# Optimization experiments

Hardware: AMD Instinct MI355X
Metric: run time of the kernel (lower is better)

## Reference

```python
import jax, jax.numpy as jnp
import numpy as np

B, C, H, W, N = 4, 128, 240, 320, 1024
LEVEL = 8.0          # scaling[0] = 4 * img_scale with img_scale=2
E1_LAMDA = 1.0
E2_LAMDA = 2.0 / 7.0
GN_LAMDA = 0.3
EPS = 1e-9


def extract_features(f, coords):
    # f: (B,C,H,W); coords: (B,N,2) float pixel coords as (x, y)
    Bf, Cf, Hf, Wf = f.shape
    x = coords[..., 0]
    y = coords[..., 1]
    x0 = jnp.floor(x)
    y0 = jnp.floor(y)
    wx = (x - x0)[:, None, :]          # (B,1,N)
    wy = (y - y0)[:, None, :]
    x0i = jnp.clip(x0.astype(jnp.int32), 0, Wf - 1)
    x1i = jnp.clip(x0i + 1, 0, Wf - 1)
    y0i = jnp.clip(y0.astype(jnp.int32), 0, Hf - 1)
    y1i = jnp.clip(y0i + 1, 0, Hf - 1)

    def g(fm, yi, xi):                 # fm: (C,H,W), yi/xi: (N,)
        return fm[:, yi, xi]           # (C,N)

    v00 = jax.vmap(g)(f, y0i, x0i)
    v01 = jax.vmap(g)(f, y0i, x1i)
    v10 = jax.vmap(g)(f, y1i, x0i)
    v11 = jax.vmap(g)(f, y1i, x1i)
    out = (v00 * (1 - wx) * (1 - wy) + v01 * wx * (1 - wy)
           + v10 * (1 - wx) * wy + v11 * wx * wy)          # (B,C,N)
    return out.transpose(0, 2, 1).reshape(Bf * coords.shape[1], Cf)


def l2_normalize(f):
    n = jnp.linalg.norm(f, axis=1, keepdims=True)
    return f / jnp.maximum(n, 1e-12)


def torch_gradient(f):
    # central differences with edge replication; gx = d/dx (width), gy = d/dy (height)
    fpx = jnp.pad(f, ((0, 0), (0, 0), (0, 0), (1, 1)), mode='edge')
    fpy = jnp.pad(f, ((0, 0), (0, 0), (1, 1), (0, 0)), mode='edge')
    gx = 0.5 * (fpx[..., 2:] - fpx[..., :-2])
    gy = 0.5 * (fpy[..., 2:, :] - fpy[..., :-2, :])
    return gx, gy


def compute_gn_loss(f_t, fb, ub, noise):
    Bn, Nn, _ = ub.shape
    xs = (2.0 * noise - 1.0) + ub                   # uniform(-1,1) jitter
    f_s = extract_features(fb, xs)
    f_t = l2_normalize(f_t)
    f_s = l2_normalize(f_s)
    r = f_s - f_t                                   # (BN, C)
    gx, gy = torch_gradient(fb)
    Jx = extract_features(gx, xs)                   # (BN, C)
    Jy = extract_features(gy, xs)
    J = jnp.stack([Jx, Jy], axis=-1)                # (BN, C, 2)
    Hm = jnp.einsum('bci,bcj->bij', J, J) + EPS * jnp.eye(2, dtype=J.dtype)
    b = jnp.einsum('bci,bc->bi', J, r)[..., None]   # (BN, 2, 1)
    # closed-form 2x2 inverse
    a = Hm[:, 0, 0]; bb = Hm[:, 0, 1]; c = Hm[:, 1, 0]; d = Hm[:, 1, 1]
    det = a * d - bb * c
    Hinv = jnp.stack([jnp.stack([d, -bb], -1),
                      jnp.stack([-c, a], -1)], -2) / det[:, None, None]
    miu = xs.reshape(Bn * Nn, 2, 1) - Hinv @ b
    diff = (ub.reshape(Bn * Nn, 2, 1) - miu)[..., 0]          # (BN, 2)
    e1 = 0.5 * jnp.sum(jnp.einsum('bi,bij,bj->b', diff, Hm, diff))
    log_det = jnp.log(det)
    e2 = Bn * Nn * jnp.log(jnp.asarray(2.0 * np.pi, dtype=det.dtype)) - 0.5 * jnp.sum(log_det)
    e = E1_LAMDA * e1 + E2_LAMDA * e2
    return e, e1, e2


def setup_inputs() -> dict:
    key = jax.random.key(0)
    k = jax.random.split(key, 7)
    F_a = jax.random.normal(k[0], (B, C, H, W), dtype=jnp.float32)
    F_b = jax.random.normal(k[1], (B, C, H, W), dtype=jnp.float32)
    # full-resolution match coords, safely inside the map after /LEVEL
    xa = jax.random.uniform(k[2], (B, N)) * (W - 5) * LEVEL + 2 * LEVEL
    ya = jax.random.uniform(k[3], (B, N)) * (H - 5) * LEVEL + 2 * LEVEL
    xb = jax.random.uniform(k[4], (B, N)) * (W - 5) * LEVEL + 2 * LEVEL
    yb = jax.random.uniform(k[5], (B, N)) * (H - 5) * LEVEL + 2 * LEVEL
    matches_a = jnp.stack([xa, ya], axis=-1)
    matches_b = jnp.stack([xb, yb], axis=-1)
    noise = jax.random.uniform(k[6], (B, N, 2), dtype=jnp.float32)
    return {"F_a": F_a, "F_b": F_b, "matches_a": matches_a,
            "matches_b": matches_b, "noise": noise}


def reference(F_a, F_b, matches_a, matches_b, noise):
    f_t = extract_features(F_a, matches_a / LEVEL)
    e, e1, e2 = compute_gn_loss(f_t, F_b, matches_b / LEVEL, noise)
    return GN_LAMDA * e, e1, e2
```

## Files before the change

### kernel.cpp

```cpp
#include <hip/hip_runtime.h>
#include <math.h>

#define B_  4
#define C_  128
#define H_  240
#define W_  320
#define N_  1024
#define NPTS (B_ * N_)
#define HW_ (H_ * W_)

__device__ __forceinline__ float wave_reduce(float v) {
    #pragma unroll
    for (int off = 32; off > 0; off >>= 1)
        v += __shfl_xor(v, off, 64);
    return v;
}

__global__ __launch_bounds__(128) void gn_point_kernel(
    const float* __restrict__ Fa, const float* __restrict__ Fb,
    const float* __restrict__ ma, const float* __restrict__ mb,
    const float* __restrict__ noise,
    float* __restrict__ ws_e1, float* __restrict__ ws_ld)
{
    const int p = blockIdx.x;
    const int b = p >> 10;
    const int c = threadIdx.x;

    const float inv_level = 1.0f / 8.0f;
    const float xa  = ma[p * 2 + 0] * inv_level;
    const float ya  = ma[p * 2 + 1] * inv_level;
    const float ubx = mb[p * 2 + 0] * inv_level;
    const float uby = mb[p * 2 + 1] * inv_level;
    const float nx  = noise[p * 2 + 0];
    const float ny  = noise[p * 2 + 1];
    const float xs  = 2.0f * nx - 1.0f + ubx;
    const float ys  = 2.0f * ny - 1.0f + uby;

    const float ax0f = floorf(xa), ay0f = floorf(ya);
    const float awx = xa - ax0f, awy = ya - ay0f;
    int ax0 = min(max((int)ax0f, 0), W_ - 1);
    int ax1 = min(ax0 + 1, W_ - 1);
    int ay0 = min(max((int)ay0f, 0), H_ - 1);
    int ay1 = min(ay0 + 1, H_ - 1);
    const float* __restrict__ fa = Fa + ((size_t)b * C_ + c) * HW_;
    const float av00 = fa[ay0 * W_ + ax0];
    const float av01 = fa[ay0 * W_ + ax1];
    const float av10 = fa[ay1 * W_ + ax0];
    const float av11 = fa[ay1 * W_ + ax1];
    const float ft = av00 * (1.f - awx) * (1.f - awy)
                   + av01 * awx * (1.f - awy)
                   + av10 * (1.f - awx) * awy
                   + av11 * awx * awy;

    const float bx0f = floorf(xs), by0f = floorf(ys);
    const float wx = xs - bx0f, wy = ys - by0f;
    int x0 = min(max((int)bx0f, 0), W_ - 1);
    int x1 = min(x0 + 1, W_ - 1);
    int y0 = min(max((int)by0f, 0), H_ - 1);
    int y1 = min(y0 + 1, H_ - 1);
    int xm = max(x0 - 1, 0);
    int xp = min(x1 + 1, W_ - 1);
    int ym = max(y0 - 1, 0);
    int yp = min(y1 + 1, H_ - 1);
    const float* __restrict__ fb = Fb + ((size_t)b * C_ + c) * HW_;

    const float r0m = fb[y0 * W_ + xm], r00 = fb[y0 * W_ + x0];
    const float r01 = fb[y0 * W_ + x1], r0p = fb[y0 * W_ + xp];
    const float r1m = fb[y1 * W_ + xm], r10 = fb[y1 * W_ + x0];
    const float r11 = fb[y1 * W_ + x1], r1p = fb[y1 * W_ + xp];
    const float rm0 = fb[ym * W_ + x0], rm1 = fb[ym * W_ + x1];
    const float rp0 = fb[yp * W_ + x0], rp1 = fb[yp * W_ + x1];

    const float w00 = (1.f - wx) * (1.f - wy);
    const float w01 = wx * (1.f - wy);
    const float w10 = (1.f - wx) * wy;
    const float w11 = wx * wy;

    const float fs = r00 * w00 + r01 * w01 + r10 * w10 + r11 * w11;
    const float jx = 0.5f * ((r01 - r0m) * w00 + (r0p - r00) * w01
                           + (r11 - r1m) * w10 + (r1p - r10) * w11);
    const float jy = 0.5f * ((r10 - rm0) * w00 + (r11 - rm1) * w01
                           + (rp0 - r00) * w10 + (rp1 - r01) * w11);

    float vals[9];
    vals[0] = ft * ft;
    vals[1] = fs * fs;
    vals[2] = jx * fs;
    vals[3] = jx * ft;
    vals[4] = jy * fs;
    vals[5] = jy * ft;
    vals[6] = jx * jx;
    vals[7] = jx * jy;
    vals[8] = jy * jy;

    #pragma unroll
    for (int k = 0; k < 9; ++k)
        vals[k] = wave_reduce(vals[k]);

    __shared__ float sm[2][9];
    const int wid = threadIdx.x >> 6;
    const int lane = threadIdx.x & 63;
    if (lane == 0) {
        #pragma unroll
        for (int k = 0; k < 9; ++k) sm[wid][k] = vals[k];
    }
    __syncthreads();

    if (threadIdx.x == 0) {
        float s[9];
        #pragma unroll
        for (int k = 0; k < 9; ++k) s[k] = sm[0][k] + sm[1][k];

        const float nt = fmaxf(sqrtf(s[0]), 1e-12f);
        const float ns = fmaxf(sqrtf(s[1]), 1e-12f);
        const float b0 = s[2] / ns - s[3] / nt;
        const float b1 = s[4] / ns - s[5] / nt;
        const float H00 = s[6] + 1e-9f;
        const float H01 = s[7];
        const float H11 = s[8] + 1e-9f;
        const float det = H00 * H11 - H01 * H01;
        const float inv = 1.0f / det;
        const float u0 = (H11 * b0 - H01 * b1) * inv;
        const float u1 = (H00 * b1 - H01 * b0) * inv;
        const float d0 = (ubx - xs) + u0;
        const float d1 = (uby - ys) + u1;
        const float quad = d0 * (H00 * d0 + H01 * d1) + d1 * (H01 * d0 + H11 * d1);
        ws_e1[p] = 0.5f * quad;
        ws_ld[p] = logf(det);
    }
}

__global__ __launch_bounds__(256) void gn_reduce_kernel(
    const float* __restrict__ ws_e1, const float* __restrict__ ws_ld,
    float* __restrict__ out)
{
    __shared__ double sm1[256];
    __shared__ double sm2[256];
    double a1 = 0.0, a2 = 0.0;
    for (int i = threadIdx.x; i < NPTS; i += 256) {
        a1 += (double)ws_e1[i];
        a2 += (double)ws_ld[i];
    }
    sm1[threadIdx.x] = a1;
    sm2[threadIdx.x] = a2;
    __syncthreads();
    for (int s = 128; s > 0; s >>= 1) {
        if (threadIdx.x < s) {
            sm1[threadIdx.x] += sm1[threadIdx.x + s];
            sm2[threadIdx.x] += sm2[threadIdx.x + s];
        }
        __syncthreads();
    }
    if (threadIdx.x == 0) {
        const double e1 = sm1[0];
        const double sum_ld = sm2[0];
        const double log2pi = (double)logf(6.283185307179586f);
        const double e2 = (double)NPTS * log2pi - 0.5 * sum_ld;
        const double e = 1.0 * e1 + (2.0 / 7.0) * e2;
        out[0] = (float)(0.3 * e);
        out[1] = (float)e1;
        out[2] = (float)e2;
    }
}

extern "C" void kernel_launch(void* const* d_in, const int* in_sizes, int n_in,
                              void* d_out, int out_size, void* d_ws, size_t ws_size,
                              hipStream_t stream) {
    const float* Fa    = (const float*)d_in[0];
    const float* Fb    = (const float*)d_in[1];
    const float* ma    = (const float*)d_in[2];
    const float* mb    = (const float*)d_in[3];
    const float* noise = (const float*)d_in[4];
    float* out = (float*)d_out;

    float* ws_e1 = (float*)d_ws;
    float* ws_ld = ws_e1 + NPTS;

    gn_point_kernel<<<NPTS, 128, 0, stream>>>(Fa, Fb, ma, mb, noise, ws_e1, ws_ld);
    gn_reduce_kernel<<<1, 256, 0, stream>>>(ws_e1, ws_ld, out);
}
```

Measured before the change: 81.89 us.

## Map one point per wavefront with two channels per lane, drop block sync

```diff
diff --git a/kernel.cpp b/kernel.cpp
--- a/kernel.cpp
+++ b/kernel.cpp
@@ -22,102 +22,119 @@
     const float* __restrict__ noise,
     float* __restrict__ ws_e1, float* __restrict__ ws_ld)
 {
-    const int p = blockIdx.x;
+    const int wid  = threadIdx.x >> 6;
+    const int lane = threadIdx.x & 63;
+    const int p = (blockIdx.x << 1) | wid;
     const int b = p >> 10;
-    const int c = threadIdx.x;
 
-    const float inv_level = 1.0f / 8.0f;
+    const float inv_level = 0.125f;
     const float xa  = ma[p * 2 + 0] * inv_level;
     const float ya  = ma[p * 2 + 1] * inv_level;
     const float ubx = mb[p * 2 + 0] * inv_level;
     const float uby = mb[p * 2 + 1] * inv_level;
-    const float nx  = noise[p * 2 + 0];
-    const float ny  = noise[p * 2 + 1];
-    const float xs  = 2.0f * nx - 1.0f + ubx;
-    const float ys  = 2.0f * ny - 1.0f + uby;
+    const float xs  = 2.0f * noise[p * 2 + 0] - 1.0f + ubx;
+    const float ys  = 2.0f * noise[p * 2 + 1] - 1.0f + uby;
 
     const float ax0f = floorf(xa), ay0f = floorf(ya);
     const float awx = xa - ax0f, awy = ya - ay0f;
-    int ax0 = min(max((int)ax0f, 0), W_ - 1);
-    int ax1 = min(ax0 + 1, W_ - 1);
-    int ay0 = min(max((int)ay0f, 0), H_ - 1);
-    int ay1 = min(ay0 + 1, H_ - 1);
-    const float* __restrict__ fa = Fa + ((size_t)b * C_ + c) * HW_;
-    const float av00 = fa[ay0 * W_ + ax0];
-    const float av01 = fa[ay0 * W_ + ax1];
-    const float av10 = fa[ay1 * W_ + ax0];
-    const float av11 = fa[ay1 * W_ + ax1];
-    const float ft = av00 * (1.f - awx) * (1.f - awy)
-                   + av01 * awx * (1.f - awy)
-                   + av10 * (1.f - awx) * awy
-                   + av11 * awx * awy;
+    const int ax0 = min(max((int)ax0f, 0), W_ - 1);
+    const int ax1 = min(ax0 + 1, W_ - 1);
+    const int ay0 = min(max((int)ay0f, 0), H_ - 1);
+    const int ay1 = min(ay0 + 1, H_ - 1);
 
     const float bx0f = floorf(xs), by0f = floorf(ys);
     const float wx = xs - bx0f, wy = ys - by0f;
-    int x0 = min(max((int)bx0f, 0), W_ - 1);
-    int x1 = min(x0 + 1, W_ - 1);
-    int y0 = min(max((int)by0f, 0), H_ - 1);
-    int y1 = min(y0 + 1, H_ - 1);
-    int xm = max(x0 - 1, 0);
-    int xp = min(x1 + 1, W_ - 1);
-    int ym = max(y0 - 1, 0);
-    int yp = min(y1 + 1, H_ - 1);
-    const float* __restrict__ fb = Fb + ((size_t)b * C_ + c) * HW_;
+    const int x0 = min(max((int)bx0f, 0), W_ - 1);
+    const int x1 = min(x0 + 1, W_ - 1);
+    const int y0 = min(max((int)by0f, 0), H_ - 1);
+    const int y1 = min(y0 + 1, H_ - 1);
+    const int xm = max(x0 - 1, 0);
+    const int xp = min(x1 + 1, W_ - 1);
+    const int ym = max(y0 - 1, 0);
+    const int yp = min(y1 + 1, H_ - 1);
 
-    const float r0m = fb[y0 * W_ + xm], r00 = fb[y0 * W_ + x0];
-    const float r01 = fb[y0 * W_ + x1], r0p = fb[y0 * W_ + xp];
-    const float r1m = fb[y1 * W_ + xm], r10 = fb[y1 * W_ + x0];
-    const float r11 = fb[y1 * W_ + x1], r1p = fb[y1 * W_ + xp];
-    const float rm0 = fb[ym * W_ + x0], rm1 = fb[ym * W_ + x1];
-    const float rp0 = fb[yp * W_ + x0], rp1 = fb[yp * W_ + x1];
+    const int o_y0 = y0 * W_, o_y1 = y1 * W_;
+    const int o_ym = ym * W_, o_yp = yp * W_;
+    const int o_a0 = ay0 * W_, o_a1 = ay1 * W_;
 
+    const size_t plane = ((size_t)b * C_ + lane) * HW_;
+    const float* __restrict__ fa0 = Fa + plane;
+    const float* __restrict__ fa1 = fa0 + (size_t)64 * HW_;
+    const float* __restrict__ fb0 = Fb + plane;
+    const float* __restrict__ fb1 = fb0 + (size_t)64 * HW_;
+
+    const float A00_0 = fa0[o_a0 + ax0], A01_0 = fa0[o_a0 + ax1];
+    const float A10_0 = fa0[o_a1 + ax0], A11_0 = fa0[o_a1 + ax1];
+    const float r0m_0 = fb0[o_y0 + xm],  r00_0 = fb0[o_y0 + x0];
+    const float r01_0 = fb0[o_y0 + x1],  r0p_0 = fb0[o_y0 + xp];
+    const float r1m_0 = fb0[o_y1 + xm],  r10_0 = fb0[o_y1 + x0];
+    const float r11_0 = fb0[o_y1 + x1],  r1p_0 = fb0[o_y1 + xp];
+    const float rm0_0 = fb0[o_ym + x0],  rm1_0 = fb0[o_ym + x1];
+    const float rp0_0 = fb0[o_yp + x0],  rp1_0 = fb0[o_yp + x1];
+
+    const float A00_1 = fa1[o_a0 + ax0], A01_1 = fa1[o_a0 + ax1];
+    const float A10_1 = fa1[o_a1 + ax0], A11_1 = fa1[o_a1 + ax1];
+    const float r0m_1 = fb1[o_y0 + xm],  r00_1 = fb1[o_y0 + x0];
+    const float r01_1 = fb1[o_y0 + x1],  r0p_1 = fb1[o_y0 + xp];
+    const float r1m_1 = fb1[o_y1 + xm],  r10_1 = fb1[o_y1 + x0];
+    const float r11_1 = fb1[o_y1 + x1],  r1p_1 = fb1[o_y1 + xp];
+    const float rm0_1 = fb1[o_ym + x0],  rm1_1 = fb1[o_ym + x1];
+    const float rp0_1 = fb1[o_yp + x0],  rp1_1 = fb1[o_yp + x1];
+
+    const float aw00 = (1.f - awx) * (1.f - awy);
+    const float aw01 = awx * (1.f - awy);
+    const float aw10 = (1.f - awx) * awy;
+    const float aw11 = awx * awy;
     const float w00 = (1.f - wx) * (1.f - wy);
     const float w01 = wx * (1.f - wy);
     const float w10 = (1.f - wx) * wy;
     const float w11 = wx * wy;
 
-    const float fs = r00 * w00 + r01 * w01 + r10 * w10 + r11 * w11;
-    const float jx = 0.5f * ((r01 - r0m) * w00 + (r0p - r00) * w01
-                           + (r11 - r1m) * w10 + (r1p - r10) * w11);
-    const float jy = 0.5f * ((r10 - rm0) * w00 + (r11 - rm1) * w01
-                           + (rp0 - r00) * w10 + (rp1 - r01) * w11);
+    float vals[9];
+    #pragma unroll
+    for (int k = 0; k < 9; ++k) vals[k] = 0.f;
 
-    float vals[9];
-    vals[0] = ft * ft;
-    vals[1] = fs * fs;
-    vals[2] = jx * fs;
-    vals[3] = jx * ft;
-    vals[4] = jy * fs;
-    vals[5] = jy * ft;
-    vals[6] = jx * jx;
-    vals[7] = jx * jy;
-    vals[8] = jy * jy;
+    #pragma unroll
+    for (int ch = 0; ch < 2; ++ch) {
+        float ft, fs, jx, jy;
+        if (ch == 0) {
+            ft = A00_0 * aw00 + A01_0 * aw01 + A10_0 * aw10 + A11_0 * aw11;
+            fs = r00_0 * w00 + r01_0 * w01 + r10_0 * w10 + r11_0 * w11;
+            jx = 0.5f * ((r01_0 - r0m_0) * w00 + (r0p_0 - r00_0) * w01
+                       + (r11_0 - r1m_0) * w10 + (r1p_0 - r10_0) * w11);
+            jy = 0.5f * ((r10_0 - rm0_0) * w00 + (r11_0 - rm1_0) * w01
+                       + (rp0_0 - r00_0) * w10 + (rp1_0 - r01_0) * w11);
+        } else {
+            ft = A00_1 * aw00 + A01_1 * aw01 + A10_1 * aw10 + A11_1 * aw11;
+            fs = r00_1 * w00 + r01_1 * w01 + r10_1 * w10 + r11_1 * w11;
+            jx = 0.5f * ((r01_1 - r0m_1) * w00 + (r0p_1 - r00_1) * w01
+                       + (r11_1 - r1m_1) * w10 + (r1p_1 - r10_1) * w11);
+            jy = 0.5f * ((r10_1 - rm0_1) * w00 + (r11_1 - rm1_1) * w01
+                       + (rp0_1 - r00_1) * w10 + (rp1_1 - r01_1) * w11);
+        }
+        vals[0] += ft * ft;
+        vals[1] += fs * fs;
+        vals[2] += jx * fs;
+        vals[3] += jx * ft;
+        vals[4] += jy * fs;
+        vals[5] += jy * ft;
+        vals[6] += jx * jx;
+        vals[7] += jx * jy;
+        vals[8] += jy * jy;
+    }
 
     #pragma unroll
     for (int k = 0; k < 9; ++k)
         vals[k] = wave_reduce(vals[k]);
 
-    __shared__ float sm[2][9];
-    const int wid = threadIdx.x >> 6;
-    const int lane = threadIdx.x & 63;
     if (lane == 0) {
-        #pragma unroll
-        for (int k = 0; k < 9; ++k) sm[wid][k] = vals[k];
-    }
-    __syncthreads();
-
-    if (threadIdx.x == 0) {
-        float s[9];
-        #pragma unroll
-        for (int k = 0; k < 9; ++k) s[k] = sm[0][k] + sm[1][k];
-
-        const float nt = fmaxf(sqrtf(s[0]), 1e-12f);
-        const float ns = fmaxf(sqrtf(s[1]), 1e-12f);
-        const float b0 = s[2] / ns - s[3] / nt;
-        const float b1 = s[4] / ns - s[5] / nt;
-        const float H00 = s[6] + 1e-9f;
-        const float H01 = s[7];
-        const float H11 = s[8] + 1e-9f;
+        const float nt = fmaxf(sqrtf(vals[0]), 1e-12f);
+        const float ns = fmaxf(sqrtf(vals[1]), 1e-12f);
+        const float b0 = vals[2] / ns - vals[3] / nt;
+        const float b1 = vals[4] / ns - vals[5] / nt;
+        const float H00 = vals[6] + 1e-9f;
+        const float H01 = vals[7];
+        const float H11 = vals[8] + 1e-9f;
         const float det = H00 * H11 - H01 * H01;
         const float inv = 1.0f / det;
         const float u0 = (H11 * b0 - H01 * b1) * inv;
@@ -176,6 +193,6 @@
     float* ws_e1 = (float*)d_ws;
     float* ws_ld = ws_e1 + NPTS;
 
-    gn_point_kernel<<<NPTS, 128, 0, stream>>>(Fa, Fb, ma, mb, noise, ws_e1, ws_ld);
+    gn_point_kernel<<<NPTS / 2, 128, 0, stream>>>(Fa, Fb, ma, mb, noise, ws_e1, ws_ld);
     gn_reduce_kernel<<<1, 256, 0, stream>>>(ws_e1, ws_ld, out);
 }
```

Result: no change. 83.48 us (+1.9%).
